# Performance work log

Measured on AMD Instinct MI355X. Metric: run time of the kernel, lower is better.

Reference implementation:

```python
import jax, jax.numpy as jnp
import numpy as np

EPS = 1e-8  # LayerNorm eps used throughout SFSRec


def _ln(x, g, b):
    m = x.mean(-1, keepdims=True)
    v = ((x - m) ** 2).mean(-1, keepdims=True)  # biased variance, as torch LayerNorm
    return (x - m) * jax.lax.rsqrt(v + EPS) * g + b


def setup_inputs() -> dict:
    key = jax.random.key(0)
    ks = jax.random.split(key, 16)
    B, L, H, V, NB = 16, 200, 256, 50000, 2
    std = 0.02  # initializer_range
    input_ids = jax.random.randint(ks[0], (B, L), 0, V + 1)
    item_emb = jax.random.normal(ks[1], (V + 1, H), jnp.float32) * std
    item_emb = item_emb.at[0].set(0.0)  # padding_idx row zeroed
    pos_emb = jax.random.normal(ks[2], (L, H), jnp.float32) * std  # maxlen == L
    emb_g = jnp.ones((H,), jnp.float32)
    emb_b = jnp.zeros((H,), jnp.float32)
    Wv = jax.random.normal(ks[3], (NB, H, H), jnp.float32) * std  # value_proj (out,in)
    Wo = jax.random.normal(ks[4], (NB, H, H), jnp.float32) * std  # out_proj (out,in)
    attn_g = jnp.ones((NB, H), jnp.float32)
    attn_b = jnp.zeros((NB, H), jnp.float32)
    W1 = jax.random.normal(ks[5], (NB, H, H), jnp.float32) * std  # conv1 kernel=1 -> linear
    b1 = jnp.zeros((NB, H), jnp.float32)
    W2 = jax.random.normal(ks[6], (NB, H, H), jnp.float32) * std
    b2 = jnp.zeros((NB, H), jnp.float32)
    ffn_g = jnp.ones((NB, H), jnp.float32)
    ffn_b = jnp.zeros((NB, H), jnp.float32)
    return {"input_ids": input_ids, "item_emb": item_emb, "pos_emb": pos_emb,
            "emb_g": emb_g, "emb_b": emb_b, "Wv": Wv, "Wo": Wo,
            "attn_g": attn_g, "attn_b": attn_b, "W1": W1, "b1": b1,
            "W2": W2, "b2": b2, "ffn_g": ffn_g, "ffn_b": ffn_b}


def reference(input_ids, item_emb, pos_emb, emb_g, emb_b, Wv, Wo,
              attn_g, attn_b, W1, b1, W2, b2, ffn_g, ffn_b):
    B, L = input_ids.shape
    H = item_emb.shape[1]
    x = item_emb[input_ids] * jnp.sqrt(jnp.float32(H)) + pos_emb[None, :, :]
    x = _ln(x, emb_g, emb_b)
    keep = (input_ids != 0)[..., None].astype(x.dtype)  # timeline mask
    x = x * keep
    # causal uniform average: T @ v == cumsum(v)/count -> O(L*H) instead of O(L^2*H)
    inv_counts = (1.0 / jnp.arange(1, L + 1, dtype=x.dtype))[None, :, None]
    NB = Wv.shape[0]
    for i in range(NB):
        v = jnp.einsum('blh,oh->blo', jnp.einsum('blh,oh->blo', x, Wv[i]), Wo[i])
        mixed = jnp.cumsum(v, axis=1) * inv_counts
        x = _ln(x + mixed, attn_g[i], attn_b[i]) * keep
        y = jax.nn.relu(jnp.einsum('blh,oh->blo', x, W1[i]) + b1[i])
        y = jnp.einsum('blh,oh->blo', y, W2[i]) + b2[i]
        x = _ln(x + y, ffn_g[i], ffn_b[i]) * keep
    # add_head: logits over all items (last_layernorm is NOT applied in the original forward)
    return jnp.einsum('blh,vh->blv', x, item_emb)
```

## Files before the change

### kernel.cpp

```cpp
#include <hip/hip_runtime.h>

#define H 256
#define LSEQ 200
#define NB 16
#define BL 3200
#define V1 50001
#define NPAD 50048

#define GAS __attribute__((address_space(1)))
#define LAS __attribute__((address_space(3)))

typedef __attribute__((ext_vector_type(8))) short short8;
typedef __attribute__((ext_vector_type(4))) float f32x4;

__device__ __forceinline__ unsigned short f2bf(float f) {
    unsigned int u = __builtin_bit_cast(unsigned int, f);
    u += 0x7fffu + ((u >> 16) & 1u);
    return (unsigned short)(u >> 16);
}


__global__ void k_f32_to_bf16(const float* __restrict__ src,
                              unsigned short* __restrict__ dst, int n) {
    int i = blockIdx.x * blockDim.x + threadIdx.x;
    if (i < n) dst[i] = f2bf(src[i]);
}

__global__ __launch_bounds__(256) void k_transpose_bf(
    const float* __restrict__ src, unsigned short* __restrict__ dst) {
    __shared__ float t[32][33];
    int i = blockIdx.z;
    int m0 = blockIdx.x * 32, h0 = blockIdx.y * 32;
    int tx = threadIdx.x & 31, ty = threadIdx.x >> 5;
#pragma unroll
    for (int s = 0; s < 32; s += 8)
        t[ty + s][tx] = src[((size_t)i * 256 + m0 + ty + s) * 256 + h0 + tx];
    __syncthreads();
#pragma unroll
    for (int s = 0; s < 32; s += 8)
        dst[((size_t)i * 256 + h0 + ty + s) * 256 + m0 + tx] = f2bf(t[tx][ty + s]);
}

__global__ void k_conv_emb(const float* __restrict__ src, unsigned short* __restrict__ dst) {
    size_t i4 = (size_t)blockIdx.x * blockDim.x + threadIdx.x;
    size_t total4 = (size_t)NPAD * H / 4;
    if (i4 >= total4) return;
    size_t e0 = i4 * 4;
    size_t row = e0 >> 8;
    ushort4 o;
    if (row < V1) {
        float4 v = *(const float4*)(src + e0);
        o.x = f2bf(v.x); o.y = f2bf(v.y); o.z = f2bf(v.z); o.w = f2bf(v.w);
    } else {
        o.x = o.y = o.z = o.w = 0;
    }
    *(ushort4*)(dst + e0) = o;
}


__device__ __forceinline__ void block_reduce2(float& s, float& ss, float* red) {
#pragma unroll
    for (int off = 32; off > 0; off >>= 1) {
        s += __shfl_down(s, off);
        ss += __shfl_down(ss, off);
    }
    int t = threadIdx.x;
    if ((t & 63) == 0) { red[(t >> 6) * 2] = s; red[(t >> 6) * 2 + 1] = ss; }
    __syncthreads();
    s  = red[0] + red[2] + red[4] + red[6];
    ss = red[1] + red[3] + red[5] + red[7];
}

__global__ __launch_bounds__(256) void k_embed_ln(
    const int* __restrict__ ids, const float* __restrict__ emb,
    const float* __restrict__ pos, const float* __restrict__ g,
    const float* __restrict__ bta, float* __restrict__ xf,
    unsigned short* __restrict__ xb) {
    __shared__ float red[8];
    int bl = blockIdx.x;
    int h = threadIdx.x;
    int l = bl % LSEQ;
    int id = ids[bl];
    float val = emb[(size_t)id * H + h] * 16.0f + pos[(size_t)l * H + h];
    float s = val, ss = val * val;
    block_reduce2(s, ss, red);
    float mean = s * (1.0f / H);
    float var = fmaxf(ss * (1.0f / H) - mean * mean, 0.0f);
    float rs = rsqrtf(var + 1e-8f);
    float keep = (id != 0) ? 1.0f : 0.0f;
    float o = ((val - mean) * rs * g[h] + bta[h]) * keep;
    xf[(size_t)bl * H + h] = o;
    xb[(size_t)bl * H + h] = f2bf(o);
}

__global__ __launch_bounds__(256) void k_add_ln(
    const float* __restrict__ x, const float* __restrict__ d,
    const float* __restrict__ g, const float* __restrict__ bta,
    const int* __restrict__ ids, float* __restrict__ xf,
    unsigned short* __restrict__ xb) {
    __shared__ float red[8];
    int bl = blockIdx.x;
    int h = threadIdx.x;
    float val = x[(size_t)bl * H + h] + d[(size_t)bl * H + h];
    float s = val, ss = val * val;
    block_reduce2(s, ss, red);
    float mean = s * (1.0f / H);
    float var = fmaxf(ss * (1.0f / H) - mean * mean, 0.0f);
    float rs = rsqrtf(var + 1e-8f);
    float keep = (ids[bl] != 0) ? 1.0f : 0.0f;
    float o = ((val - mean) * rs * g[h] + bta[h]) * keep;
    xf[(size_t)bl * H + h] = o;
    xb[(size_t)bl * H + h] = f2bf(o);
}

__global__ __launch_bounds__(64) void k_cumsum(float* __restrict__ v) {
    int b = blockIdx.x;
    int h = blockIdx.y * 64 + threadIdx.x;
    float* p = v + (size_t)b * LSEQ * H + h;
    float acc = 0.0f;
    for (int l = 0; l < LSEQ; l += 4) {
        float a0 = p[(size_t)(l + 0) * H];
        float a1 = p[(size_t)(l + 1) * H];
        float a2 = p[(size_t)(l + 2) * H];
        float a3 = p[(size_t)(l + 3) * H];
        acc += a0; p[(size_t)(l + 0) * H] = acc * (1.0f / (float)(l + 1));
        acc += a1; p[(size_t)(l + 1) * H] = acc * (1.0f / (float)(l + 2));
        acc += a2; p[(size_t)(l + 2) * H] = acc * (1.0f / (float)(l + 3));
        acc += a3; p[(size_t)(l + 3) * H] = acc * (1.0f / (float)(l + 4));
    }
}

template<int BIAS, int RELU, int WF32, int WBF16>
__global__ __launch_bounds__(256) void k_gemm64(
    const unsigned short* __restrict__ A,
    const unsigned short* __restrict__ Bmat,
    const float* __restrict__ bias,
    float* __restrict__ outF,
    unsigned short* __restrict__ outB,
    int N, int K) {
    int bm = blockIdx.x * 64;
    int bn = blockIdx.y * 64;
    int tid = threadIdx.x;
    int w = tid >> 6, l = tid & 63;
    int wr = (w >> 1) * 32, wc = (w & 1) * 32;
    int l16 = l & 15, lk = (l >> 4) * 8;

    const unsigned short* Ap = A + (size_t)(bm + wr + l16) * K + lk;
    const unsigned short* Bp = Bmat + (size_t)(bn + wc + l16) * K + lk;

    f32x4 acc00 = {0.f,0.f,0.f,0.f}, acc01 = {0.f,0.f,0.f,0.f};
    f32x4 acc10 = {0.f,0.f,0.f,0.f}, acc11 = {0.f,0.f,0.f,0.f};

#pragma unroll
    for (int k0 = 0; k0 < 256; k0 += 32) {
        short8 a0 = *(const short8*)(Ap + k0);
        short8 a1 = *(const short8*)(Ap + (size_t)16 * K + k0);
        short8 b0 = *(const short8*)(Bp + k0);
        short8 b1 = *(const short8*)(Bp + (size_t)16 * K + k0);
        acc00 = __builtin_amdgcn_mfma_f32_16x16x32_bf16(a0, b0, acc00, 0, 0, 0);
        acc01 = __builtin_amdgcn_mfma_f32_16x16x32_bf16(a0, b1, acc01, 0, 0, 0);
        acc10 = __builtin_amdgcn_mfma_f32_16x16x32_bf16(a1, b0, acc10, 0, 0, 0);
        acc11 = __builtin_amdgcn_mfma_f32_16x16x32_bf16(a1, b1, acc11, 0, 0, 0);
    }

    int r0 = (l >> 4) * 4;
#pragma unroll
    for (int i = 0; i < 2; ++i) {
#pragma unroll
        for (int j = 0; j < 2; ++j) {
            f32x4 a = (i == 0) ? (j == 0 ? acc00 : acc01) : (j == 0 ? acc10 : acc11);
            int col = bn + wc + j * 16 + l16;
            float bv = BIAS ? bias[col] : 0.0f;
            int rowb = bm + wr + i * 16 + r0;
#pragma unroll
            for (int r = 0; r < 4; ++r) {
                float vv = a[r] + bv;
                if (RELU) vv = fmaxf(vv, 0.0f);
                size_t idx = (size_t)(rowb + r) * N + col;
                if (WF32) outF[idx] = vv;
                if (WBF16) outB[idx] = f2bf(vv);
            }
        }
    }
}

#define LGM 25
#define LGN 391
#define LGWG (LGM * LGN)

__global__ __launch_bounds__(256, 2) void k_logits(
    const unsigned short* __restrict__ A,
    const unsigned short* __restrict__ B,
    float* __restrict__ out) {
    __shared__ unsigned short lB[128 * 256];

    int orig = blockIdx.x;
    int q = LGWG >> 3, r = LGWG & 7;
    int xcd = orig & 7, sub = orig >> 3;
    int wg = (xcd < r ? xcd * (q + 1) : r * (q + 1) + (xcd - r) * q) + sub;
    int mi = wg % LGM, ni = wg / LGM;
    int bm = mi * 128, bn = ni * 128;

    int tid = threadIdx.x;
    int w = tid >> 6, l = tid & 63;
    int wr = (w >> 1) * 64, wc = (w & 1) * 64;
    int l16 = l & 15, lc = l >> 4;

#pragma unroll
    for (int it = 0; it < 16; ++it) {
        int idx = it * 256 + tid;
        int row = idx >> 5;
        int cd = idx & 31;
        int cs = cd ^ (row & 7);
        const unsigned short* g = B + (size_t)(bn + row) * 256 + cs * 8;
        unsigned short* lp = &lB[(idx & ~63) * 8];
        __builtin_amdgcn_global_load_lds((const GAS unsigned int*)g,
                                         (LAS unsigned int*)lp, 16, 0, 0);
    }

    short8 af[8][4];
#pragma unroll
    for (int kt = 0; kt < 8; ++kt)
#pragma unroll
        for (int i = 0; i < 4; ++i)
            af[kt][i] = *(const short8*)(A + (size_t)(bm + wr + i * 16 + l16) * 256
                                           + kt * 32 + lc * 8);

    __syncthreads();

    f32x4 acc[4][4] = {};
#pragma unroll
    for (int kt = 0; kt < 8; ++kt) {
        short8 bf[4];
#pragma unroll
        for (int j = 0; j < 4; ++j) {
            int row = wc + j * 16 + l16;
            int pc = (kt * 4 + lc) ^ (row & 7);
            bf[j] = *(const short8*)&lB[row * 256 + pc * 8];
        }
#pragma unroll
        for (int i = 0; i < 4; ++i)
#pragma unroll
            for (int j = 0; j < 4; ++j)
                acc[i][j] = __builtin_amdgcn_mfma_f32_16x16x32_bf16(
                    af[kt][i], bf[j], acc[i][j], 0, 0, 0);
    }

#pragma unroll
    for (int i = 0; i < 4; ++i) {
        int mrow = bm + wr + i * 16 + lc * 4;
#pragma unroll
        for (int j = 0; j < 4; ++j) {
            int n = bn + wc + j * 16 + l16;
            if (n < V1) {
#pragma unroll
                for (int rg = 0; rg < 4; ++rg)
                    out[(size_t)(mrow + rg) * V1 + n] = acc[i][j][rg];
            }
        }
    }
}


extern "C" void kernel_launch(void* const* d_in, const int* in_sizes, int n_in,
                              void* d_out, int out_size, void* d_ws, size_t ws_size,
                              hipStream_t stream) {
    const int*   ids      = (const int*)d_in[0];
    const float* item_emb = (const float*)d_in[1];
    const float* pos_emb  = (const float*)d_in[2];
    const float* emb_g    = (const float*)d_in[3];
    const float* emb_b    = (const float*)d_in[4];
    const float* Wv       = (const float*)d_in[5];
    const float* Wo       = (const float*)d_in[6];
    const float* attn_g   = (const float*)d_in[7];
    const float* attn_b   = (const float*)d_in[8];
    const float* W1       = (const float*)d_in[9];
    const float* b1       = (const float*)d_in[10];
    const float* W2       = (const float*)d_in[11];
    const float* b2       = (const float*)d_in[12];
    const float* ffn_g    = (const float*)d_in[13];
    const float* ffn_b    = (const float*)d_in[14];
    float* out = (float*)d_out;

    char* ws = (char*)d_ws;
    size_t off = 0;
    auto alloc = [&](size_t bytes) -> void* {
        void* p = ws + off;
        off += (bytes + 255) & ~(size_t)255;
        return p;
    };
    float* xf  = (float*)alloc((size_t)BL * H * 4);
    float* vbuf= (float*)alloc((size_t)BL * H * 4);
    float* y2  = (float*)alloc((size_t)BL * H * 4);
    unsigned short* xb  = (unsigned short*)alloc((size_t)BL * H * 2);
    unsigned short* y1b = (unsigned short*)alloc((size_t)BL * H * 2);
    unsigned short* WcB = (unsigned short*)alloc((size_t)2 * H * H * 2);
    unsigned short* W1B = (unsigned short*)alloc((size_t)2 * H * H * 2);
    unsigned short* W2B = (unsigned short*)alloc((size_t)2 * H * H * 2);
    unsigned short* WoB = (unsigned short*)alloc((size_t)2 * H * H * 2);
    unsigned short* WvT = (unsigned short*)alloc((size_t)2 * H * H * 2);
    unsigned short* embB= (unsigned short*)alloc((size_t)NPAD * H * 2);

    k_f32_to_bf16<<<dim3(512), dim3(256), 0, stream>>>(W1, W1B, 2 * H * H);
    k_f32_to_bf16<<<dim3(512), dim3(256), 0, stream>>>(W2, W2B, 2 * H * H);
    k_f32_to_bf16<<<dim3(512), dim3(256), 0, stream>>>(Wo, WoB, 2 * H * H);
    k_transpose_bf<<<dim3(8, 8, 2), dim3(256), 0, stream>>>(Wv, WvT);
    {
        int n4 = NPAD * H / 4;
        k_conv_emb<<<dim3((n4 + 255) / 256), dim3(256), 0, stream>>>(item_emb, embB);
    }
    for (int i = 0; i < 2; ++i)
        k_gemm64<0,0,0,1><<<dim3(4, 4), dim3(256), 0, stream>>>(
            WoB + (size_t)i * H * H, WvT + (size_t)i * H * H, nullptr,
            nullptr, WcB + (size_t)i * H * H, H, H);

    k_embed_ln<<<dim3(BL), dim3(H), 0, stream>>>(ids, item_emb, pos_emb, emb_g, emb_b, xf, xb);

    for (int i = 0; i < 2; ++i) {
        k_gemm64<0,0,1,0><<<dim3(BL / 64, H / 64), dim3(256), 0, stream>>>(
            xb, WcB + (size_t)i * H * H, nullptr, vbuf, nullptr, H, H);
        k_cumsum<<<dim3(NB, 4), dim3(64), 0, stream>>>(vbuf);
        k_add_ln<<<dim3(BL), dim3(H), 0, stream>>>(
            xf, vbuf, attn_g + (size_t)i * H, attn_b + (size_t)i * H, ids, xf, xb);
        k_gemm64<1,1,0,1><<<dim3(BL / 64, H / 64), dim3(256), 0, stream>>>(
            xb, W1B + (size_t)i * H * H, b1 + (size_t)i * H, nullptr, y1b, H, H);
        k_gemm64<1,0,1,0><<<dim3(BL / 64, H / 64), dim3(256), 0, stream>>>(
            y1b, W2B + (size_t)i * H * H, b2 + (size_t)i * H, y2, nullptr, H, H);
        k_add_ln<<<dim3(BL), dim3(H), 0, stream>>>(
            xf, y2, ffn_g + (size_t)i * H, ffn_b + (size_t)i * H, ids, xf, xb);
    }

    k_logits<<<dim3(LGWG), dim3(256), 0, stream>>>(xb, embB, out);
}
```

Before: 447.3 us.

## Keep item-embedding strip in registers and loop over row tiles in logits kernel

The logits GEMM now assigns each block a 64-column strip of the item table, held in registers for the whole block, plus half of the row tiles. The block loops over those row tiles, streaming A from global/L2, in place of loading a 128x256 B tile into LDS per 128x128 output tile. This removes the LDS staging and sync, frees LDS so occupancy can rise (launch bounds raised to 3), and cuts the work-group count. In exchange each block does a long serial loop with more A re-reads, drops the XCD-aware remapping, and still needs the launch grid set to match the new block count (shown only partly).

```diff
diff --git a/kernel.cpp b/kernel.cpp
--- a/kernel.cpp
+++ b/kernel.cpp
@@ -184,78 +184,61 @@
     }
 }
 
-#define LGM 25
-#define LGN 391
-#define LGWG (LGM * LGN)
-
-__global__ __launch_bounds__(256, 2) void k_logits(
+#define LGSTRIPS 782
+#define LGWG (LGSTRIPS * 2)
+
+__global__ __launch_bounds__(256, 3) void k_logits(
     const unsigned short* __restrict__ A,
     const unsigned short* __restrict__ B,
     float* __restrict__ out) {
-    __shared__ unsigned short lB[128 * 256];
-
-    int orig = blockIdx.x;
-    int q = LGWG >> 3, r = LGWG & 7;
-    int xcd = orig & 7, sub = orig >> 3;
-    int wg = (xcd < r ? xcd * (q + 1) : r * (q + 1) + (xcd - r) * q) + sub;
-    int mi = wg % LGM, ni = wg / LGM;
-    int bm = mi * 128, bn = ni * 128;
+    int bid = blockIdx.x;
+    int strip = bid >> 1, half = bid & 1;
+    int n0 = strip * 64;
+    int mt0 = half ? 13 : 0;
+    int mt1 = half ? 25 : 13;
 
     int tid = threadIdx.x;
     int w = tid >> 6, l = tid & 63;
-    int wr = (w >> 1) * 64, wc = (w & 1) * 64;
+    int wr = (w >> 1) * 64;
+    int wc = (w & 1) * 32;
     int l16 = l & 15, lc = l >> 4;
 
-#pragma unroll
-    for (int it = 0; it < 16; ++it) {
-        int idx = it * 256 + tid;
-        int row = idx >> 5;
-        int cd = idx & 31;
-        int cs = cd ^ (row & 7);
-        const unsigned short* g = B + (size_t)(bn + row) * 256 + cs * 8;
-        unsigned short* lp = &lB[(idx & ~63) * 8];
-        __builtin_amdgcn_global_load_lds((const GAS unsigned int*)g,
-                                         (LAS unsigned int*)lp, 16, 0, 0);
-    }
-
-    short8 af[8][4];
+    short8 breg[8][2];
 #pragma unroll
     for (int kt = 0; kt < 8; ++kt)
 #pragma unroll
-        for (int i = 0; i < 4; ++i)
-            af[kt][i] = *(const short8*)(A + (size_t)(bm + wr + i * 16 + l16) * 256
-                                           + kt * 32 + lc * 8);
-
-    __syncthreads();
-
-    f32x4 acc[4][4] = {};
-#pragma unroll
-    for (int kt = 0; kt < 8; ++kt) {
-        short8 bf[4];
-#pragma unroll
-        for (int j = 0; j < 4; ++j) {
-            int row = wc + j * 16 + l16;
-            int pc = (kt * 4 + lc) ^ (row & 7);
-            bf[j] = *(const short8*)&lB[row * 256 + pc * 8];
+        for (int j = 0; j < 2; ++j)
+            breg[kt][j] = *(const short8*)(
+                B + (size_t)(n0 + wc + j * 16 + l16) * 256 + kt * 32 + lc * 8);
+
+    for (int mt = mt0; mt < mt1; ++mt) {
+        int bm = mt * 128;
+        const unsigned short* Abase = A + (size_t)(bm + wr + l16) * 256 + lc * 8;
+        f32x4 acc[4][2] = {};
+#pragma unroll
+        for (int kt = 0; kt < 8; ++kt) {
+            short8 af[4];
+#pragma unroll
+            for (int i = 0; i < 4; ++i)
+                af[i] = *(const short8*)(Abase + (size_t)(i * 16) * 256 + kt * 32);
+#pragma unroll
+            for (int i = 0; i < 4; ++i)
+#pragma unroll
+                for (int j = 0; j < 2; ++j)
+                    acc[i][j] = __builtin_amdgcn_mfma_f32_16x16x32_bf16(
+                        af[i], breg[kt][j], acc[i][j], 0, 0, 0);
         }
 #pragma unroll
-        for (int i = 0; i < 4; ++i)
-#pragma unroll
-            for (int j = 0; j < 4; ++j)
-                acc[i][j] = __builtin_amdgcn_mfma_f32_16x16x32_bf16(
-                    af[kt][i], bf[j], acc[i][j], 0, 0, 0);
-    }
-
-#pragma unroll
-    for (int i = 0; i < 4; ++i) {
-        int mrow = bm + wr + i * 16 + lc * 4;
-#pragma unroll
-        for (int j = 0; j < 4; ++j) {
-            int n = bn + wc + j * 16 + l16;
-            if (n < V1) {
-#pragma unroll
-                for (int rg = 0; rg < 4; ++rg)
-                    out[(size_t)(mrow + rg) * V1 + n] = acc[i][j][rg];
+        for (int i = 0; i < 4; ++i) {
+            int mrow = bm + wr + i * 16 + lc * 4;
+#pragma unroll
+            for (int j = 0; j < 2; ++j) {
+                int n = n0 + wc + j * 16 + l16;
+                if (n < V1) {
+#pragma unroll
+                    for (int rg = 0; rg < 4; ++rg)
+                        out[(size_t)(mrow + rg) * V1 + n] = acc[i][j][rg];
+                }
             }
         }
     }
```

Result: slower. 659.7 us (+47.5%).
